# Kernel tuning notes

Measured on AMD Instinct MI355X. Metric: run time of the kernel, lower is better.

The kernel has to match this reference:

```python
import jax, jax.numpy as jnp
import numpy as np

NX, NY = 128, 128
NT = 50
DECAY = 0.1
M1 = M2 = 12
WIDTH = 64


def _spectral(x, w1, w2):
    # x: [B, W, NX, NY]; w1/w2: complex [W, W, M1, M2]
    xf = jnp.fft.rfft2(x)                                   # [B, W, NX, NY//2+1]
    of = jnp.zeros(xf.shape[:2] + (NX, NY // 2 + 1), jnp.complex64)
    of = of.at[:, :, :M1, :M2].set(jnp.einsum('bixy,ioxy->boxy', xf[:, :, :M1, :M2], w1))
    of = of.at[:, :, NX - M1:, :M2].set(jnp.einsum('bixy,ioxy->boxy', xf[:, :, NX - M1:, :M2], w2))
    return jnp.fft.irfft2(of, s=(NX, NY))


def _forward(xyt_q, obs_coords, obs_vals, x_grid, y_grid,
             fc0_w, fc0_b, spec_w1r, spec_w1i, spec_w2r, spec_w2i,
             pw_w, pw_b, fc1_w, fc1_b, fc2_w, fc2_b,
             nb_idx, sensor_iy, sensor_ix, Lx, Ly):
    B, K = nb_idx.shape
    # ---- gather obs, temporal-decay weight, scatter-add into sparse grid ----
    sensor_ids = nb_idx // NT                               # [B, K]
    t_nb = obs_coords[nb_idx, 2]                            # [B, K]
    w = jnp.exp(-DECAY * jnp.abs(t_nb - xyt_q[:, None, 2])) # [B, K]
    vals = obs_vals[nb_idx] * w                             # [B, K]
    lin = sensor_iy[sensor_ids] * NY + sensor_ix[sensor_ids]
    flat = (lin + jnp.arange(B)[:, None] * (NX * NY)).ravel()
    sparse = jnp.zeros(B * NX * NY, obs_vals.dtype).at[flat].add(vals.ravel())
    counts = jnp.zeros(B * NX * NY, obs_vals.dtype).at[flat].add(w.ravel())
    grid = jnp.where(counts > 0, sparse / jnp.maximum(counts, 1e-6), 0.0).reshape(B, NX, NY)
    # ---- FNO core ----
    inp = jnp.stack([grid,
                     jnp.broadcast_to(x_grid, (B, NX, NY)),
                     jnp.broadcast_to(y_grid, (B, NX, NY))], axis=1)  # [B, 3, NX, NY]
    x = jnp.einsum('bcxy,cw->bwxy', inp, fc0_w) + fc0_b[None, :, None, None]
    for i in range(4):
        y = (_spectral(x, spec_w1r[i] + 1j * spec_w1i[i], spec_w2r[i] + 1j * spec_w2i[i])
             + jnp.einsum('bcxy,oc->boxy', x, pw_w[i]) + pw_b[i][None, :, None, None])
        x = jax.nn.gelu(y, approximate=False) if i < 3 else y
    h = jax.nn.gelu(jnp.einsum('bwxy,wf->bxyf', x, fc1_w) + fc1_b, approximate=False)
    field = (jnp.einsum('bxyf,fo->bxyo', h, fc2_w) + fc2_b).transpose(0, 3, 1, 2)  # [B, 3, NX, NY]
    # ---- bilinear sample at query points ----
    x01 = jnp.clip(xyt_q[:, 0] / max(Lx, 1e-6), 0.0, 1.0)
    y01 = jnp.clip(xyt_q[:, 1] / max(Ly, 1e-6), 0.0, 1.0)
    gx = x01 * (NX - 1)
    gy = y01 * (NY - 1)
    x0 = jnp.floor(gx).astype(jnp.int32)
    y0 = jnp.floor(gy).astype(jnp.int32)
    x1 = jnp.minimum(x0 + 1, NX - 1)
    y1 = jnp.minimum(y0 + 1, NY - 1)
    wx = (gx - x0)[:, None]
    wy = (gy - y0)[:, None]
    b = jnp.arange(B)
    f00 = field[b, :, x0, y0]
    f10 = field[b, :, x1, y0]
    f01 = field[b, :, x0, y1]
    f11 = field[b, :, x1, y1]
    top = f00 * (1.0 - wx) + f10 * wx
    bot = f01 * (1.0 - wx) + f11 * wx
    return top * (1.0 - wy) + bot * wy                       # [B, 3]


def setup_inputs() -> dict:
    key = jax.random.key(0)
    ks = jax.random.split(key, 20)
    B, K, NOBS, NS = 64, 64, 50000, 1000
    scale = 1.0 / (WIDTH * WIDTH)
    inp = {
        'xyt_q': jax.random.uniform(ks[0], (B, 3), jnp.float32),
        'obs_coords': jax.random.uniform(ks[1], (NOBS, 3), jnp.float32),
        'obs_vals': jax.random.normal(ks[2], (NOBS,), jnp.float32),
        'x_grid': jax.random.uniform(ks[3], (NX, NY), jnp.float32),
        'y_grid': jax.random.uniform(ks[4], (NX, NY), jnp.float32),
        'fc0_w': jax.random.normal(ks[5], (3, WIDTH), jnp.float32) * 0.3,
        'fc0_b': jnp.zeros((WIDTH,), jnp.float32),
        'spec_w1r': scale * jax.random.uniform(ks[6], (4, WIDTH, WIDTH, M1, M2), jnp.float32),
        'spec_w1i': scale * jax.random.uniform(ks[7], (4, WIDTH, WIDTH, M1, M2), jnp.float32),
        'spec_w2r': scale * jax.random.uniform(ks[8], (4, WIDTH, WIDTH, M1, M2), jnp.float32),
        'spec_w2i': scale * jax.random.uniform(ks[9], (4, WIDTH, WIDTH, M1, M2), jnp.float32),
        'pw_w': jax.random.normal(ks[10], (4, WIDTH, WIDTH), jnp.float32) * (1.0 / np.sqrt(WIDTH)),
        'pw_b': jnp.zeros((4, WIDTH), jnp.float32),
        'fc1_w': jax.random.normal(ks[11], (WIDTH, 128), jnp.float32) * (1.0 / np.sqrt(WIDTH)),
        'fc1_b': jnp.zeros((128,), jnp.float32),
        'fc2_w': jax.random.normal(ks[12], (128, 3), jnp.float32) * (1.0 / np.sqrt(128.0)),
        'fc2_b': jnp.zeros((3,), jnp.float32),
        'nb_idx': jax.random.randint(ks[13], (B, K), 0, NOBS, jnp.int32),
        'sensor_iy': jax.random.randint(ks[14], (NS,), 0, NX, jnp.int32),
        'sensor_ix': jax.random.randint(ks[15], (NS,), 0, NY, jnp.int32),
        'Lx': 1,
        'Ly': 1,
    }
    return inp


def reference(xyt_q, obs_coords, obs_vals, x_grid, y_grid,
              fc0_w, fc0_b, spec_w1r, spec_w1i, spec_w2r, spec_w2i,
              pw_w, pw_b, fc1_w, fc1_b, fc2_w, fc2_b,
              nb_idx, sensor_iy, sensor_ix, Lx, Ly):
    return _forward(xyt_q, obs_coords, obs_vals, x_grid, y_grid,
                    fc0_w, fc0_b, spec_w1r, spec_w1i, spec_w2r, spec_w2i,
                    pw_w, pw_b, fc1_w, fc1_b, fc2_w, fc2_b,
                    nb_idx, sensor_iy, sensor_ix, Lx, Ly)
```

## Files before the change

### kernel.cpp

```cpp
#include <hip/hip_runtime.h>
#include <math.h>

#define NXg 128
#define NYg 128
#define Pg  (NXg*NYg)
#define Bq  64
#define Wd  64
#define NKX 24
#define NMODE (NKX*12)
#define PI2_128 0.04908738521234052f

typedef _Float16 f16x8 __attribute__((ext_vector_type(8)));
typedef _Float16 f16x4 __attribute__((ext_vector_type(4)));
typedef float    f32x4 __attribute__((ext_vector_type(4)));

#define OFF_TC  0
#define OFF_TS  (OFF_TC + 128)
#define F32_END (OFF_TS + 128)
#define H_T1E  0
#define H_T1ET (H_T1E + 32*128)
#define H_A2   (H_T1ET + 128*32)
#define H_PWH  (H_A2 + 48*256)
#define H_T2ET (H_PWH + 4*64*64)
#define H_XFHR (H_T2ET + 128*64)
#define H_XFHI (H_XFHR + 288*4096)
#define H_OFHR (H_XFHI + 288*4096)
#define H_OFHI (H_OFHR + 288*4096)
#define H_WHR  (H_OFHI + 288*4096)
#define H_WHI  (H_WHR + (size_t)4*288*4096)
#define H_YG   (H_WHI + (size_t)4*288*4096)
#define H_X    (H_YG + (size_t)Bq*Wd*128*24)
#define H_U    (H_X + (size_t)Bq*128*128*64)

__device__ __forceinline__ float fast_gelu(float v) {
    float a = fabsf(v) * 0.70710678118654752f;
    float t = 1.f / (1.f + 0.3275911f * a);
    float p = t * (0.254829592f + t * (-0.284496736f + t * (1.421413741f +
              t * (-1.453152027f + t * 1.061405429f))));
    float er = 1.f - p * __expf(-a * a);
    er = copysignf(er, v);
    return 0.5f * v * (1.f + er);
}

__global__ void k_prep(_Float16* T1e_g, _Float16* T1eT_g, _Float16* A2_g,
                       const float* pww, _Float16* PWh, _Float16* T2eT_g,
                       float* Tc, float* Ts,
                       const float* xyt, const float* obs_c, const float* obs_v,
                       const int* nb, const int* siy, const int* six,
                       float* val, float* cnt,
                       const float* w1r, const float* w1i,
                       const float* w2r, const float* w2i,
                       _Float16* Whr, _Float16* Whi) {
    int blk = blockIdx.x;
    if (blk < 64) {
        int t = blk * 256 + threadIdx.x;
        if (t < 32*128) {
            int r = t >> 7, y = t & 127;
            float v = 0.f;
            if (r < 12)      v =  cosf((float)((r * y) & 127) * PI2_128);
            else if (r < 24) v = -sinf((float)(((r-12) * y) & 127) * PI2_128);
            T1e_g[t] = (_Float16)v;
            int y2 = t >> 5, r2 = t & 31;
            float v2 = 0.f;
            if (r2 < 12)      v2 =  cosf((float)((r2 * y2) & 127) * PI2_128);
            else if (r2 < 24) v2 = -sinf((float)(((r2-12) * y2) & 127) * PI2_128);
            T1eT_g[t] = (_Float16)v2;
        }
        if (t < 48*256) {
            int m = t >> 8, k = t & 255;
            int x = k & 127;
            int hi = (k >= 128);
            float v;
            if (m < 24) {
                int kx = (m < 12) ? m : (104 + m);
                float th = (float)((kx * x) & 127) * PI2_128;
                v = hi ? sinf(th) : cosf(th);
            } else {
                int mm = m - 24;
                int kx = (mm < 12) ? mm : (104 + mm);
                float th = (float)((kx * x) & 127) * PI2_128;
                v = hi ? cosf(th) : -sinf(th);
            }
            A2_g[t] = (_Float16)v;
        }
        if (t < 4*64*64) PWh[t] = (_Float16)pww[t];
        if (t < 128*64) {
            int x = t >> 6, k = t & 63;
            float v = 0.f;
            if (k < 24) {
                int kx = (k < 12) ? k : (104 + k);
                v = cosf((float)((kx * x) & 127) * PI2_128);
            } else if (k < 48) {
                int kk = k - 24;
                int kx = (kk < 12) ? kk : (104 + kk);
                v = sinf((float)((kx * x) & 127) * PI2_128);
            }
            T2eT_g[t] = (_Float16)v;
        }
        if (t < 128) {
            float th = (float)t * PI2_128;
            Tc[t] = cosf(th);
            Ts[t] = sinf(th);
        }
    } else if (blk < 80) {
        int t = (blk - 64) * 256 + threadIdx.x;
        int b = t >> 6;
        int id = nb[t];
        int sid = id / 50;
        float tq = xyt[b*3 + 2];
        float w = expf(-0.1f * fabsf(obs_c[id*3 + 2] - tq));
        int lin = siy[sid] * NYg + six[sid];
        atomicAdd(&val[b*Pg + lin], obs_v[id] * w);
        atomicAdd(&cnt[b*Pg + lin], w);
    } else {
        int u = blk - 80;
        int layer = u / 288, mode = u - layer*288;
        int kxi = mode / 12, ky = mode - kxi*12;
        const float *wr, *wi; int kxw;
        if (kxi < 12) { wr = w1r; wi = w1i; kxw = kxi; }
        else          { wr = w2r; wi = w2i; kxw = kxi - 12; }
        size_t obase = (size_t)(layer*288 + mode) * 4096;
        size_t lbase = (size_t)layer * 64*64*144 + (size_t)kxw*12 + ky;
        for (int k = 0; k < 16; k++) {
            int p = k*256 + threadIdx.x;
            int o = p >> 6, i = p & 63;
            size_t widx = lbase + (size_t)(i*64 + o)*144;
            Whr[obase + p] = (_Float16)wr[widx];
            Whi[obase + p] = (_Float16)wi[widx];
        }
    }
}

__device__ __forceinline__ void stageA(const _Float16 (*Xn)[76], const _Float16* __restrict__ T1e_g,
                                       _Float16* __restrict__ Yg, int b, int row, int tid) {
    int wave = tid >> 6, lane = tid & 63;
    int l15 = lane & 15, quad = lane >> 4;
    f16x8 bf[8];
    #pragma unroll
    for (int u = 0; u < 8; u++) {
        int nt2 = u >> 2, q = u & 3;
        bf[u] = *(const f16x8*)&T1e_g[(nt2*16 + l15)*128 + q*32 + quad*8];
    }
    f16x8 af[4];
    #pragma unroll
    for (int q = 0; q < 4; q++)
        #pragma unroll
        for (int j = 0; j < 8; j++)
            af[q][j] = Xn[q*32 + quad*8 + j][wave*16 + l15];
    #pragma unroll
    for (int nt2 = 0; nt2 < 2; nt2++) {
        f32x4 acc = {0.f,0.f,0.f,0.f};
        #pragma unroll
        for (int q = 0; q < 4; q++)
            acc = __builtin_amdgcn_mfma_f32_16x16x32_f16(af[q], bf[nt2*4 + q], acc, 0, 0, 0);
        int t = nt2*16 + l15;
        if (t < 24) {
            #pragma unroll
            for (int r = 0; r < 4; r++) {
                int o = wave*16 + quad*4 + r;
                Yg[((size_t)(b*64 + o)*128 + row)*24 + t] = (_Float16)acc[r];
            }
        }
    }
}

__global__ __launch_bounds__(256) void k_fc0y(const float* __restrict__ val, const float* __restrict__ cnt,
                      const float* __restrict__ xg, const float* __restrict__ yg,
                      const float* __restrict__ w, const float* __restrict__ bb,
                      const _Float16* __restrict__ T1e_g,
                      _Float16* __restrict__ Yg) {
    __shared__ _Float16 Xn[128][76];
    __shared__ float wl[4][64];
    int row = blockIdx.x, b = blockIdx.y;
    int tid = threadIdx.x;
    if (tid < 64) {
        wl[0][tid] = w[tid]; wl[1][tid] = w[64+tid]; wl[2][tid] = w[128+tid]; wl[3][tid] = bb[tid];
    }
    __syncthreads();
    {
        int y = tid & 127, half = tid >> 7;
        int p = row*128 + y;
        float c = cnt[(size_t)b*Pg + p];
        float g = (c > 0.f) ? val[(size_t)b*Pg + p] / fmaxf(c, 1e-6f) : 0.f;
        float a1 = xg[p], a2 = yg[p];
        #pragma unroll
        for (int blk = 0; blk < 4; blk++) {
            f16x8 pk;
            #pragma unroll
            for (int j = 0; j < 8; j++) {
                int o = half*32 + blk*8 + j;
                pk[j] = (_Float16)(g*wl[0][o] + a1*wl[1][o] + a2*wl[2][o] + wl[3][o]);
            }
            *(f16x8*)&Xn[y][half*32 + blk*8] = pk;
        }
    }
    __syncthreads();
    stageA(Xn, T1e_g, Yg, b, row, tid);
}

__global__ __launch_bounds__(256) void k_sB(const _Float16* __restrict__ Yg,
                    const _Float16* __restrict__ A2_g,
                    _Float16* __restrict__ xfhr, _Float16* __restrict__ xfhi) {
    __shared__ _Float16 Ys[28][136];
    int bc = blockIdx.x;
    int tid = threadIdx.x;
    int wave = tid >> 6, lane = tid & 63;
    int l15 = lane & 15, quad = lane >> 4;
    const _Float16* base = Yg + (size_t)bc * 3072;
    for (int i = tid; i < 3072; i += 256) {
        int x = i / 24, t = i - x*24;
        Ys[t][x] = base[i];
    }
    __syncthreads();
    if (wave < 3) {
        f32x4 acc = {0.f,0.f,0.f,0.f};
        #pragma unroll
        for (int q = 0; q < 8; q++) {
            f16x8 a = *(const f16x8*)&A2_g[(size_t)(wave*16 + l15)*256 + q*32 + quad*8];
            const _Float16* brow = (q < 4) ? &Ys[l15][q*32 + quad*8]
                                           : &Ys[12 + l15][(q-4)*32 + quad*8];
            f16x8 bfr = *(const f16x8*)brow;
            acc = __builtin_amdgcn_mfma_f32_16x16x32_f16(a, bfr, acc, 0, 0, 0);
        }
        if (l15 < 12) {
            #pragma unroll
            for (int r = 0; r < 4; r++) {
                int m = wave*16 + quad*4 + r;
                if (m < 24) xfhr[(size_t)(m*12 + l15)*4096 + bc] = (_Float16)acc[r];
                else        xfhi[(size_t)((m-24)*12 + l15)*4096 + bc] = (_Float16)acc[r];
            }
        }
    }
}

__global__ __launch_bounds__(256) void k_s3m(const _Float16* __restrict__ xfhr, const _Float16* __restrict__ xfhi,
                    const _Float16* __restrict__ Whr, const _Float16* __restrict__ Whi,
                    _Float16* __restrict__ ofhr, _Float16* __restrict__ ofhi, int layer) {
    __shared__ _Float16 Xr[64][72], Xi[64][72];
    int mode = blockIdx.x;
    int tid = threadIdx.x;
    int wave = tid >> 6, lane = tid & 63;
    int l15 = lane & 15, quad = lane >> 4;
    const _Float16* pr = xfhr + (size_t)mode * 4096;
    const _Float16* pi = xfhi + (size_t)mode * 4096;
    for (int c8 = tid; c8 < 512; c8 += 256) {
        int b = c8 >> 3, seg = c8 & 7;
        *(f16x8*)&Xr[b][seg*8] = *(const f16x8*)&pr[c8*8];
        *(f16x8*)&Xi[b][seg*8] = *(const f16x8*)&pi[c8*8];
    }
    __syncthreads();
    size_t wb = ((size_t)(layer*288 + mode)*64 + wave*16 + l15) * 64 + quad*8;
    f16x8 wr0 = *(const f16x8*)&Whr[wb];
    f16x8 wr1 = *(const f16x8*)&Whr[wb + 32];
    f16x8 wi0 = *(const f16x8*)&Whi[wb];
    f16x8 wi1 = *(const f16x8*)&Whi[wb + 32];
    #pragma unroll
    for (int mt = 0; mt < 4; mt++) {
        f16x8 xr0 = *(const f16x8*)&Xr[mt*16 + l15][quad*8];
        f16x8 xr1 = *(const f16x8*)&Xr[mt*16 + l15][32 + quad*8];
        f16x8 xi0 = *(const f16x8*)&Xi[mt*16 + l15][quad*8];
        f16x8 xi1 = *(const f16x8*)&Xi[mt*16 + l15][32 + quad*8];
        f16x8 xn0, xn1;
        #pragma unroll
        for (int j = 0; j < 8; j++) { xn0[j] = -xi0[j]; xn1[j] = -xi1[j]; }
        f32x4 cr = {0.f,0.f,0.f,0.f}, ci = {0.f,0.f,0.f,0.f};
        cr = __builtin_amdgcn_mfma_f32_16x16x32_f16(xr0, wr0, cr, 0, 0, 0);
        cr = __builtin_amdgcn_mfma_f32_16x16x32_f16(xr1, wr1, cr, 0, 0, 0);
        cr = __builtin_amdgcn_mfma_f32_16x16x32_f16(xn0, wi0, cr, 0, 0, 0);
        cr = __builtin_amdgcn_mfma_f32_16x16x32_f16(xn1, wi1, cr, 0, 0, 0);
        ci = __builtin_amdgcn_mfma_f32_16x16x32_f16(xr0, wi0, ci, 0, 0, 0);
        ci = __builtin_amdgcn_mfma_f32_16x16x32_f16(xr1, wi1, ci, 0, 0, 0);
        ci = __builtin_amdgcn_mfma_f32_16x16x32_f16(xi0, wr0, ci, 0, 0, 0);
        ci = __builtin_amdgcn_mfma_f32_16x16x32_f16(xi1, wr1, ci, 0, 0, 0);
        #pragma unroll
        for (int r = 0; r < 4; r++) {
            int b = mt*16 + quad*4 + r;
            int o = wave*16 + l15;
            ofhr[(size_t)mode*4096 + b*64 + o] = (_Float16)cr[r];
            ofhi[(size_t)mode*4096 + b*64 + o] = (_Float16)ci[r];
        }
    }
}

__global__ __launch_bounds__(256) void k_sG(const _Float16* __restrict__ ofhr, const _Float16* __restrict__ ofhi,
                    const _Float16* __restrict__ T2eT_g, _Float16* __restrict__ Gh) {
    __shared__ _Float16 As[64][72];
    __shared__ _Float16 Cs[128][72];
    int b = blockIdx.x, t = blockIdx.y;
    int tid = threadIdx.x;
    int wave = tid >> 6, lane = tid & 63;
    int l15 = lane & 15, quad = lane >> 4;
    int ky = (t < 12) ? t : (t - 12);
    float sc = ((ky == 0) ? 1.f : 2.f) * (1.f/16384.f);
    bool isReal = (t < 12);
    for (int i = tid; i < 1536; i += 256) {
        int kxi = i >> 6, o = i & 63;
        size_t idx = (size_t)(kxi*12 + ky)*4096 + b*64 + o;
        float vr = (float)ofhr[idx] * sc, vi = (float)ofhi[idx] * sc;
        As[o][kxi]      = (_Float16)(isReal ? vr : vi);
        As[o][24 + kxi] = (_Float16)(isReal ? -vi : vr);
    }
    for (int i = tid; i < 1024; i += 256)
        As[i >> 4][48 + (i & 15)] = (_Float16)0.f;
    __syncthreads();
    f16x8 a0 = *(const f16x8*)&As[wave*16 + l15][quad*8];
    f16x8 a1 = *(const f16x8*)&As[wave*16 + l15][32 + quad*8];
    #pragma unroll
    for (int nt = 0; nt < 8; nt++) {
        f16x8 b0 = *(const f16x8*)&T2eT_g[(nt*16 + l15)*64 + quad*8];
        f16x8 b1 = *(const f16x8*)&T2eT_g[(nt*16 + l15)*64 + 32 + quad*8];
        f32x4 acc = {0.f,0.f,0.f,0.f};
        acc = __builtin_amdgcn_mfma_f32_16x16x32_f16(a0, b0, acc, 0, 0, 0);
        acc = __builtin_amdgcn_mfma_f32_16x16x32_f16(a1, b1, acc, 0, 0, 0);
        f16x4 pk;
        #pragma unroll
        for (int r = 0; r < 4; r++) pk[r] = (_Float16)acc[r];
        *(f16x4*)&Cs[nt*16 + l15][wave*16 + quad*4] = pk;
    }
    __syncthreads();
    _Float16* outp = Gh + ((size_t)(b*24 + t) << 13);
    float4* o4 = (float4*)outp;
    for (int i = tid; i < 1024; i += 256) {
        int x = i >> 3, seg = i & 7;
        o4[i] = *(const float4*)&Cs[x][seg*8];
    }
}

__global__ __launch_bounds__(256) void k_s45(_Float16* __restrict__ xh,
                    const _Float16* __restrict__ Gh,
                    const _Float16* __restrict__ T1e_g, const _Float16* __restrict__ T1eT_g,
                    const _Float16* __restrict__ PWh,
                    const float* __restrict__ pwb,
                    _Float16* __restrict__ Yg, int layer,
                    const float* __restrict__ xyt, const int* __restrict__ Lx,
                    const float* __restrict__ val, const float* __restrict__ cnt,
                    const float* __restrict__ xg, const float* __restrict__ yg,
                    const float* __restrict__ fc0w, const float* __restrict__ fc0b) {
    __shared__ _Float16 BsT[128][76];
    __shared__ float wl[4][64];
    int row = blockIdx.x, b = blockIdx.y;
    int tid = threadIdx.x;
    int wave = tid >> 6, lane = tid & 63;
    int l15 = lane & 15, quad = lane >> 4;

    _Float16* xrow = xh + (size_t)(b*128 + row) * 8192;

    f16x8 af0 = *(const f16x8*)&PWh[(size_t)(layer*64 + wave*16 + l15)*64 + quad*8];
    f16x8 af1 = *(const f16x8*)&PWh[(size_t)(layer*64 + wave*16 + l15)*64 + 32 + quad*8];
    f16x8 af2;
    #pragma unroll
    for (int j = 0; j < 8; j++) af2[j] = (_Float16)0.f;
    if (quad < 3) {
        const _Float16* gbase = Gh + ((size_t)(b*24 + quad*8)*128 + row)*64 + wave*16 + l15;
        #pragma unroll
        for (int j = 0; j < 8; j++) af2[j] = gbase[(size_t)j * 8192];
    }
    f16x8 b2a[8];
    #pragma unroll
    for (int nt = 0; nt < 8; nt++)
        b2a[nt] = *(const f16x8*)&T1eT_g[(nt*16 + l15)*32 + quad*8];
    float pb[4];
    #pragma unroll
    for (int r = 0; r < 4; r++)
        pb[r] = pwb[layer*64 + wave*16 + quad*4 + r];

    if (layer == 0) {
        if (tid < 64) {
            wl[0][tid] = fc0w[tid]; wl[1][tid] = fc0w[64+tid];
            wl[2][tid] = fc0w[128+tid]; wl[3][tid] = fc0b[tid];
        }
        __syncthreads();
        int y = tid & 127, half = tid >> 7;
        int p = row*128 + y;
        float c = cnt[(size_t)b*Pg + p];
        float g = (c > 0.f) ? val[(size_t)b*Pg + p] / fmaxf(c, 1e-6f) : 0.f;
        float a1 = xg[p], a2 = yg[p];
        #pragma unroll
        for (int blk = 0; blk < 4; blk++) {
            f16x8 pk;
            #pragma unroll
            for (int j = 0; j < 8; j++) {
                int o = half*32 + blk*8 + j;
                pk[j] = (_Float16)(g*wl[0][o] + a1*wl[1][o] + a2*wl[2][o] + wl[3][o]);
            }
            *(f16x8*)&BsT[y][half*32 + blk*8] = pk;
        }
    } else {
        const float4* xr4 = (const float4*)xrow;
        for (int i = tid; i < 1024; i += 256) {
            int y = i >> 3, seg = i & 7;
            *(float4*)&BsT[y][seg*8] = xr4[i];
        }
    }
    __syncthreads();

    f32x4 acc[8];
    #pragma unroll
    for (int nt = 0; nt < 8; nt++) {
        f32x4 a = {0.f,0.f,0.f,0.f};
        f16x8 b0 = *(const f16x8*)&BsT[nt*16 + l15][quad*8];
        f16x8 b1 = *(const f16x8*)&BsT[nt*16 + l15][32 + quad*8];
        a = __builtin_amdgcn_mfma_f32_16x16x32_f16(af0, b0, a, 0, 0, 0);
        a = __builtin_amdgcn_mfma_f32_16x16x32_f16(af1, b1, a, 0, 0, 0);
        a = __builtin_amdgcn_mfma_f32_16x16x32_f16(af2, b2a[nt], a, 0, 0, 0);
        acc[nt] = a;
    }
    __syncthreads();

    #pragma unroll
    for (int nt = 0; nt < 8; nt++) {
        int y = nt*16 + l15;
        f16x4 pk;
        #pragma unroll
        for (int r = 0; r < 4; r++) {
            float v = acc[nt][r] + pb[r];
            pk[r] = (_Float16)fast_gelu(v);
        }
        *(f16x4*)&BsT[y][wave*16 + quad*4] = pk;
    }
    __syncthreads();

    bool store_x = true;
    if (layer == 2) {
        float Lxf = fmaxf((float)Lx[0], 1e-6f);
        float x01 = fminf(fmaxf(xyt[b*3 + 0] / Lxf, 0.f), 1.f);
        float gxp = x01 * (NXg - 1);
        int x0 = (int)floorf(gxp);
        int x1 = min(x0 + 1, NXg - 1);
        store_x = (row == x0) || (row == x1);
    }
    if (store_x) {
        float4* xw4 = (float4*)xrow;
        for (int i = tid; i < 1024; i += 256) {
            int y = i >> 3, seg = i & 7;
            xw4[i] = *(const float4*)&BsT[y][seg*8];
        }
    }
    stageA(BsT, T1e_g, Yg, b, row, tid);
}

__global__ __launch_bounds__(256) void k_final(const _Float16* __restrict__ x,
                    const _Float16* __restrict__ ofhr, const _Float16* __restrict__ ofhi,
                    const float* __restrict__ pw, const float* __restrict__ pwb,
                    const float* __restrict__ fc1w, const float* __restrict__ fc1b,
                    const float* __restrict__ fc2w, const float* __restrict__ fc2b,
                    const float* __restrict__ xyt, const int* __restrict__ Lx, const int* __restrict__ Ly,
                    const float* __restrict__ Tc, const float* __restrict__ Ts,
                    float* __restrict__ out) {
    __shared__ float y4[4][64];
    __shared__ float hh[4][129];
    __shared__ int   pxy[4][2];
    __shared__ float wxy[2];
    __shared__ float tc[128], ts[128];
    int b = blockIdx.x;
    if (threadIdx.x < 128) {
        tc[threadIdx.x] = Tc[threadIdx.x];
        ts[threadIdx.x] = Ts[threadIdx.x];
    }
    if (threadIdx.x == 0) {
        float Lxf = fmaxf((float)Lx[0], 1e-6f);
        float Lyf = fmaxf((float)Ly[0], 1e-6f);
        float x01 = fminf(fmaxf(xyt[b*3 + 0] / Lxf, 0.f), 1.f);
        float y01 = fminf(fmaxf(xyt[b*3 + 1] / Lyf, 0.f), 1.f);
        float gx = x01 * (NXg - 1), gy = y01 * (NYg - 1);
        int x0 = (int)floorf(gx), y0 = (int)floorf(gy);
        int x1 = min(x0 + 1, NXg - 1), y1 = min(y0 + 1, NYg - 1);
        wxy[0] = gx - (float)x0;
        wxy[1] = gy - (float)y0;
        pxy[0][0] = x0; pxy[0][1] = y0;
        pxy[1][0] = x1; pxy[1][1] = y0;
        pxy[2][0] = x0; pxy[2][1] = y1;
        pxy[3][0] = x1; pxy[3][1] = y1;
    }
    __syncthreads();
    {
        int p = threadIdx.x >> 6, o = threadIdx.x & 63;
        int px = pxy[p][0], py = pxy[p][1];
        float gkr[12], gki[12];
        #pragma unroll
        for (int ky = 0; ky < 12; ky++) { gkr[ky] = 0.f; gki[ky] = 0.f; }
        for (int kxi = 0; kxi < 24; kxi++) {
            int kx = (kxi < 12) ? kxi : (104 + kxi);
            int m = (kx * px) & 127;
            float cc = tc[m], ss = ts[m];
            #pragma unroll
            for (int ky = 0; ky < 12; ky++) {
                size_t idx = (size_t)(kxi*12 + ky)*4096 + b*64 + o;
                float a = (float)ofhr[idx], bb = (float)ofhi[idx];
                gkr[ky] += a*cc - bb*ss;
                gki[ky] += a*ss + bb*cc;
            }
        }
        float sp = gkr[0];
        #pragma unroll
        for (int ky = 1; ky < 12; ky++) {
            int m = (ky * py) & 127;
            sp += 2.f * (gkr[ky]*tc[m] - gki[ky]*ts[m]);
        }
        float s = 0.f;
        const _Float16* xb = x + ((size_t)(b*128 + px)*128 + py)*64;
        #pragma unroll 4
        for (int c = 0; c < 64; c++)
            s += pw[3*4096 + o*64 + c] * (float)xb[c];
        y4[p][o] = sp * (1.f/16384.f) + s + pwb[3*64 + o];
    }
    __syncthreads();
    for (int i = threadIdx.x; i < 512; i += 256) {
        int p = i >> 7, f = i & 127;
        float s = fc1b[f];
        #pragma unroll 4
        for (int w = 0; w < 64; w++) s += y4[p][w] * fc1w[w*128 + f];
        hh[p][f] = 0.5f * s * (1.f + erff(s * 0.70710678118654752f));
    }
    __syncthreads();
    if (threadIdx.x < 3) {
        int o3 = threadIdx.x;
        float f4[4];
        #pragma unroll
        for (int p = 0; p < 4; p++) {
            float s = fc2b[o3];
            #pragma unroll 4
            for (int f = 0; f < 128; f++) s += hh[p][f] * fc2w[f*3 + o3];
            f4[p] = s;
        }
        float wx = wxy[0], wy = wxy[1];
        float top = f4[0]*(1.f - wx) + f4[1]*wx;
        float bot = f4[2]*(1.f - wx) + f4[3]*wx;
        out[b*3 + o3] = top*(1.f - wy) + bot*wy;
    }
}

extern "C" void kernel_launch(void* const* d_in, const int* in_sizes, int n_in,
                              void* d_out, int out_size, void* d_ws, size_t ws_size,
                              hipStream_t stream) {
    const float* xyt    = (const float*)d_in[0];
    const float* obs_c  = (const float*)d_in[1];
    const float* obs_v  = (const float*)d_in[2];
    const float* xg     = (const float*)d_in[3];
    const float* yg     = (const float*)d_in[4];
    const float* fc0w   = (const float*)d_in[5];
    const float* fc0b   = (const float*)d_in[6];
    const float* w1r    = (const float*)d_in[7];
    const float* w1i    = (const float*)d_in[8];
    const float* w2r    = (const float*)d_in[9];
    const float* w2i    = (const float*)d_in[10];
    const float* pww    = (const float*)d_in[11];
    const float* pwb    = (const float*)d_in[12];
    const float* fc1w   = (const float*)d_in[13];
    const float* fc1b   = (const float*)d_in[14];
    const float* fc2w   = (const float*)d_in[15];
    const float* fc2b   = (const float*)d_in[16];
    const int*   nb     = (const int*)d_in[17];
    const int*   siy    = (const int*)d_in[18];
    const int*   six    = (const int*)d_in[19];
    const int*   Lx     = (const int*)d_in[20];
    const int*   Ly     = (const int*)d_in[21];
    float* out = (float*)d_out;

    float* W = (float*)d_ws;
    float* Tc  = W + OFF_TC;
    float* Ts  = W + OFF_TS;
    _Float16* Hbase = (_Float16*)(W + F32_END);
    _Float16* T1e_g  = Hbase + H_T1E;
    _Float16* T1eT_g = Hbase + H_T1ET;
    _Float16* A2_g   = Hbase + H_A2;
    _Float16* PWh    = Hbase + H_PWH;
    _Float16* T2eT_g = Hbase + H_T2ET;
    _Float16* xfhr   = Hbase + H_XFHR;
    _Float16* xfhi   = Hbase + H_XFHI;
    _Float16* ofhr   = Hbase + H_OFHR;
    _Float16* ofhi   = Hbase + H_OFHI;
    _Float16* Whr    = Hbase + H_WHR;
    _Float16* Whi    = Hbase + H_WHI;
    _Float16* Yg     = Hbase + H_YG;
    _Float16* xh     = Hbase + H_X;
    float*    val    = (float*)(Hbase + H_U);
    float*    cnt    = val + Bq*Pg;
    _Float16* Gh     = Hbase + H_U;
    _Float16* Gh2    = Hbase + H_U + (size_t)4*Bq*Pg;

    hipMemsetAsync(val, 0, (size_t)2 * Bq * Pg * sizeof(float), stream);

    k_prep<<<1232, 256, 0, stream>>>(T1e_g, T1eT_g, A2_g, pww, PWh, T2eT_g, Tc, Ts,
                                     xyt, obs_c, obs_v, nb, siy, six, val, cnt,
                                     w1r, w1i, w2r, w2i, Whr, Whi);
    k_fc0y<<<dim3(128, Bq), 256, 0, stream>>>(val, cnt, xg, yg, fc0w, fc0b, T1e_g, Yg);

    for (int l = 0; l < 3; l++) {
        k_sB<<<Bq*Wd, 256, 0, stream>>>(Yg, A2_g, xfhr, xfhi);
        k_s3m<<<288, 256, 0, stream>>>(xfhr, xfhi, Whr, Whi, ofhr, ofhi, l);
        k_sG<<<dim3(Bq, 24), 256, 0, stream>>>(ofhr, ofhi, T2eT_g, Gh2);
        k_s45<<<dim3(128, Bq), 256, 0, stream>>>(xh, Gh2, T1e_g, T1eT_g, PWh, pwb, Yg, l,
                                                 xyt, Lx, val, cnt, xg, yg, fc0w, fc0b);
    }
    k_sB<<<Bq*Wd, 256, 0, stream>>>(Yg, A2_g, xfhr, xfhi);
    k_s3m<<<288, 256, 0, stream>>>(xfhr, xfhi, Whr, Whi, ofhr, ofhi, 3);
    k_final<<<Bq, 256, 0, stream>>>(xh, ofhr, ofhi, pww, pwb, fc1w, fc1b, fc2w, fc2b,
                                    xyt, Lx, Ly, Tc, Ts, out);
}
```

Baseline: 745.0 us.

## Process two rows per block in k_s45 and tile spectral weight repack via LDS

k_s45 now handles two grid rows per block, loading the T1e DFT fragments and PW weights once and reusing them across both rows. Results are written to global memory straight from registers instead of through a shared-memory round trip, and the grid is halved. The k_prep weight-conversion path is restructured to stage one output channel's 64x144 slab in LDS, so global reads become coalesced and writes are transposed. This trades higher LDS and register use per block (launch bounds set to 3 blocks per CU) for less redundant loading.

```diff
diff --git a/kernel.cpp b/kernel.cpp
--- a/kernel.cpp
+++ b/kernel.cpp
@@ -51,6 +51,7 @@
                        const float* w1r, const float* w1i,
                        const float* w2r, const float* w2i,
                        _Float16* Whr, _Float16* Whi) {
+    __shared__ _Float16 L[64][146];
     int blk = blockIdx.x;
     if (blk < 64) {
         int t = blk * 256 + threadIdx.x;
@@ -114,33 +115,38 @@
         atomicAdd(&cnt[b*Pg + lin], w);
     } else {
         int u = blk - 80;
-        int layer = u / 288, mode = u - layer*288;
-        int kxi = mode / 12, ky = mode - kxi*12;
-        const float *wr, *wi; int kxw;
-        if (kxi < 12) { wr = w1r; wi = w1i; kxw = kxi; }
-        else          { wr = w2r; wi = w2i; kxw = kxi - 12; }
-        size_t obase = (size_t)(layer*288 + mode) * 4096;
-        size_t lbase = (size_t)layer * 64*64*144 + (size_t)kxw*12 + ky;
-        for (int k = 0; k < 16; k++) {
-            int p = k*256 + threadIdx.x;
-            int o = p >> 6, i = p & 63;
-            size_t widx = lbase + (size_t)(i*64 + o)*144;
-            Whr[obase + p] = (_Float16)wr[widx];
-            Whi[obase + p] = (_Float16)wi[widx];
-        }
-    }
-}
-
-__device__ __forceinline__ void stageA(const _Float16 (*Xn)[76], const _Float16* __restrict__ T1e_g,
-                                       _Float16* __restrict__ Yg, int b, int row, int tid) {
-    int wave = tid >> 6, lane = tid & 63;
+        int layer = u >> 8;
+        int rem = u & 255;
+        int o = rem & 63, ri = (rem >> 6) & 1, half = rem >> 7;
+        const float* src = half ? (ri ? w2i : w2r) : (ri ? w1i : w1r);
+        _Float16* dst = ri ? Whi : Whr;
+        size_t sbase = (size_t)layer * 589824 + (size_t)o * 144;
+        for (int idx = threadIdx.x; idx < 9216; idx += 256) {
+            int i = idx / 144, m = idx - i*144;
+            L[i][m] = (_Float16)src[sbase + (size_t)i*9216 + m];
+        }
+        __syncthreads();
+        size_t obase = ((size_t)(layer*288 + half*144) << 12) + o*64;
+        for (int idx = threadIdx.x; idx < 9216; idx += 256) {
+            int m = idx >> 6, i = idx & 63;
+            dst[obase + ((size_t)m << 12) + i] = L[i][m];
+        }
+    }
+}
+
+__device__ __forceinline__ void stageA_bf(const _Float16* __restrict__ T1e_g, int lane, f16x8* bf) {
     int l15 = lane & 15, quad = lane >> 4;
-    f16x8 bf[8];
     #pragma unroll
     for (int u = 0; u < 8; u++) {
         int nt2 = u >> 2, q = u & 3;
         bf[u] = *(const f16x8*)&T1e_g[(nt2*16 + l15)*128 + q*32 + quad*8];
     }
+}
+
+__device__ __forceinline__ void stageA_core(const _Float16 (*Xn)[76], const f16x8* bf,
+                                            _Float16* __restrict__ Yg, int b, int row, int tid) {
+    int wave = tid >> 6, lane = tid & 63;
+    int l15 = lane & 15, quad = lane >> 4;
     f16x8 af[4];
     #pragma unroll
     for (int q = 0; q < 4; q++)
@@ -162,6 +168,13 @@
             }
         }
     }
+}
+
+__device__ __forceinline__ void stageA(const _Float16 (*Xn)[76], const _Float16* __restrict__ T1e_g,
+                                       _Float16* __restrict__ Yg, int b, int row, int tid) {
+    f16x8 bf[8];
+    stageA_bf(T1e_g, tid & 63, bf);
+    stageA_core(Xn, bf, Yg, b, row, tid);
 }
 
 __global__ __launch_bounds__(256) void k_fc0y(const float* __restrict__ val, const float* __restrict__ cnt,
@@ -326,7 +339,7 @@
     }
 }
 
-__global__ __launch_bounds__(256) void k_s45(_Float16* __restrict__ xh,
+__global__ __launch_bounds__(256, 3) void k_s45(_Float16* __restrict__ xh,
                     const _Float16* __restrict__ Gh,
                     const _Float16* __restrict__ T1e_g, const _Float16* __restrict__ T1eT_g,
                     const _Float16* __restrict__ PWh,
@@ -336,25 +349,30 @@
                     const float* __restrict__ val, const float* __restrict__ cnt,
                     const float* __restrict__ xg, const float* __restrict__ yg,
                     const float* __restrict__ fc0w, const float* __restrict__ fc0b) {
-    __shared__ _Float16 BsT[128][76];
+    __shared__ _Float16 BsT[2][128][76];
     __shared__ float wl[4][64];
-    int row = blockIdx.x, b = blockIdx.y;
+    int rp = blockIdx.x, b = blockIdx.y;
+    int row0 = rp << 1;
     int tid = threadIdx.x;
     int wave = tid >> 6, lane = tid & 63;
     int l15 = lane & 15, quad = lane >> 4;
 
-    _Float16* xrow = xh + (size_t)(b*128 + row) * 8192;
+    f16x8 af2[2];
+    #pragma unroll
+    for (int r2 = 0; r2 < 2; r2++)
+        #pragma unroll
+        for (int j = 0; j < 8; j++) af2[r2][j] = (_Float16)0.f;
+    if (quad < 3) {
+        #pragma unroll
+        for (int r2 = 0; r2 < 2; r2++) {
+            const _Float16* gbase = Gh + ((size_t)(b*24 + quad*8)*128 + row0 + r2)*64 + wave*16 + l15;
+            #pragma unroll
+            for (int j = 0; j < 8; j++) af2[r2][j] = gbase[(size_t)j * 8192];
+        }
+    }
 
     f16x8 af0 = *(const f16x8*)&PWh[(size_t)(layer*64 + wave*16 + l15)*64 + quad*8];
     f16x8 af1 = *(const f16x8*)&PWh[(size_t)(layer*64 + wave*16 + l15)*64 + 32 + quad*8];
-    f16x8 af2;
-    #pragma unroll
-    for (int j = 0; j < 8; j++) af2[j] = (_Float16)0.f;
-    if (quad < 3) {
-        const _Float16* gbase = Gh + ((size_t)(b*24 + quad*8)*128 + row)*64 + wave*16 + l15;
-        #pragma unroll
-        for (int j = 0; j < 8; j++) af2[j] = gbase[(size_t)j * 8192];
-    }
     f16x8 b2a[8];
     #pragma unroll
     for (int nt = 0; nt < 8; nt++)
@@ -371,72 +389,84 @@
         }
         __syncthreads();
         int y = tid & 127, half = tid >> 7;
-        int p = row*128 + y;
-        float c = cnt[(size_t)b*Pg + p];
-        float g = (c > 0.f) ? val[(size_t)b*Pg + p] / fmaxf(c, 1e-6f) : 0.f;
-        float a1 = xg[p], a2 = yg[p];
-        #pragma unroll
-        for (int blk = 0; blk < 4; blk++) {
-            f16x8 pk;
+        #pragma unroll
+        for (int r2 = 0; r2 < 2; r2++) {
+            int p = (row0 + r2)*128 + y;
+            float c = cnt[(size_t)b*Pg + p];
+            float g = (c > 0.f) ? val[(size_t)b*Pg + p] / fmaxf(c, 1e-6f) : 0.f;
+            float a1 = xg[p], a2 = yg[p];
             #pragma unroll
-            for (int j = 0; j < 8; j++) {
-                int o = half*32 + blk*8 + j;
-                pk[j] = (_Float16)(g*wl[0][o] + a1*wl[1][o] + a2*wl[2][o] + wl[3][o]);
-            }
-            *(f16x8*)&BsT[y][half*32 + blk*8] = pk;
+            for (int blk = 0; blk < 4; blk++) {
+                f16x8 pkk;
+                #pragma unroll
+                for (int j = 0; j < 8; j++) {
+                    int o = half*32 + blk*8 + j;
+                    pkk[j] = (_Float16)(g*wl[0][o] + a1*wl[1][o] + a2*wl[2][o] + wl[3][o]);
+                }
+                *(f16x8*)&BsT[r2][y][half*32 + blk*8] = pkk;
+            }
         }
     } else {
-        const float4* xr4 = (const float4*)xrow;
-        for (int i = tid; i < 1024; i += 256) {
-            int y = i >> 3, seg = i & 7;
-            *(float4*)&BsT[y][seg*8] = xr4[i];
-        }
-    }
-    __syncthreads();
-
-    f32x4 acc[8];
-    #pragma unroll
-    for (int nt = 0; nt < 8; nt++) {
-        f32x4 a = {0.f,0.f,0.f,0.f};
-        f16x8 b0 = *(const f16x8*)&BsT[nt*16 + l15][quad*8];
-        f16x8 b1 = *(const f16x8*)&BsT[nt*16 + l15][32 + quad*8];
-        a = __builtin_amdgcn_mfma_f32_16x16x32_f16(af0, b0, a, 0, 0, 0);
-        a = __builtin_amdgcn_mfma_f32_16x16x32_f16(af1, b1, a, 0, 0, 0);
-        a = __builtin_amdgcn_mfma_f32_16x16x32_f16(af2, b2a[nt], a, 0, 0, 0);
-        acc[nt] = a;
-    }
-    __syncthreads();
-
-    #pragma unroll
-    for (int nt = 0; nt < 8; nt++) {
-        int y = nt*16 + l15;
-        f16x4 pk;
-        #pragma unroll
-        for (int r = 0; r < 4; r++) {
-            float v = acc[nt][r] + pb[r];
-            pk[r] = (_Float16)fast_gelu(v);
-        }
-        *(f16x4*)&BsT[y][wave*16 + quad*4] = pk;
-    }
-    __syncthreads();
-
-    bool store_x = true;
+        #pragma unroll
+        for (int r2 = 0; r2 < 2; r2++) {
+            const float4* xr4 = (const float4*)(xh + (size_t)(b*128 + row0 + r2) * 8192);
+            for (int i = tid; i < 1024; i += 256) {
+                int y = i >> 3, seg = i & 7;
+                *(float4*)&BsT[r2][y][seg*8] = xr4[i];
+            }
+        }
+    }
+    __syncthreads();
+
+    f16x4 pk[2][8];
+    #pragma unroll
+    for (int r2 = 0; r2 < 2; r2++) {
+        f32x4 acc[8];
+        #pragma unroll
+        for (int nt = 0; nt < 8; nt++) {
+            f32x4 a = {0.f,0.f,0.f,0.f};
+            f16x8 b0 = *(const f16x8*)&BsT[r2][nt*16 + l15][quad*8];
+            f16x8 b1 = *(const f16x8*)&BsT[r2][nt*16 + l15][32 + quad*8];
+            a = __builtin_amdgcn_mfma_f32_16x16x32_f16(af0, b0, a, 0, 0, 0);
+            a = __builtin_amdgcn_mfma_f32_16x16x32_f16(af1, b1, a, 0, 0, 0);
+            a = __builtin_amdgcn_mfma_f32_16x16x32_f16(af2[r2], b2a[nt], a, 0, 0, 0);
+            acc[nt] = a;
+        }
+        #pragma unroll
+        for (int nt = 0; nt < 8; nt++)
+            #pragma unroll
+            for (int r = 0; r < 4; r++)
+                pk[r2][nt][r] = (_Float16)fast_gelu(acc[nt][r] + pb[r]);
+    }
+    __syncthreads();
+
+    bool st[2] = {true, true};
     if (layer == 2) {
         float Lxf = fmaxf((float)Lx[0], 1e-6f);
         float x01 = fminf(fmaxf(xyt[b*3 + 0] / Lxf, 0.f), 1.f);
         float gxp = x01 * (NXg - 1);
         int x0 = (int)floorf(gxp);
         int x1 = min(x0 + 1, NXg - 1);
-        store_x = (row == x0) || (row == x1);
-    }
-    if (store_x) {
-        float4* xw4 = (float4*)xrow;
-        for (int i = tid; i < 1024; i += 256) {
-            int y = i >> 3, seg = i & 7;
-            xw4[i] = *(const float4*)&BsT[y][seg*8];
-        }
-    }
-    stageA(BsT, T1e_g, Yg, b, row, tid);
+        st[0] = (row0 == x0) || (row0 == x1);
+        st[1] = (row0 + 1 == x0) || (row0 + 1 == x1);
+    }
+    #pragma unroll
+    for (int r2 = 0; r2 < 2; r2++) {
+        _Float16* xrow = xh + (size_t)(b*128 + row0 + r2) * 8192;
+        #pragma unroll
+        for (int nt = 0; nt < 8; nt++) {
+            int y = nt*16 + l15;
+            *(f16x4*)&BsT[r2][y][wave*16 + quad*4] = pk[r2][nt];
+            if (st[r2])
+                *(f16x4*)&xrow[(size_t)y*64 + wave*16 + quad*4] = pk[r2][nt];
+        }
+    }
+    __syncthreads();
+
+    f16x8 bf[8];
+    stageA_bf(T1e_g, lane, bf);
+    stageA_core(BsT[0], bf, Yg, b, row0, tid);
+    stageA_core(BsT[1], bf, Yg, b, row0 + 1, tid);
 }
 
 __global__ __launch_bounds__(256) void k_final(const _Float16* __restrict__ x,
@@ -576,12 +606,11 @@
     _Float16* xh     = Hbase + H_X;
     float*    val    = (float*)(Hbase + H_U);
     float*    cnt    = val + Bq*Pg;
-    _Float16* Gh     = Hbase + H_U;
     _Float16* Gh2    = Hbase + H_U + (size_t)4*Bq*Pg;
 
     hipMemsetAsync(val, 0, (size_t)2 * Bq * Pg * sizeof(float), stream);
 
-    k_prep<<<1232, 256, 0, stream>>>(T1e_g, T1eT_g, A2_g, pww, PWh, T2eT_g, Tc, Ts,
+    k_prep<<<1104, 256, 0, stream>>>(T1e_g, T1eT_g, A2_g, pww, PWh, T2eT_g, Tc, Ts,
                                      xyt, obs_c, obs_v, nb, siy, six, val, cnt,
                                      w1r, w1i, w2r, w2i, Whr, Whi);
     k_fc0y<<<dim3(128, Bq), 256, 0, stream>>>(val, cnt, xg, yg, fc0w, fc0b, T1e_g, Yg);
@@ -590,8 +619,8 @@
         k_sB<<<Bq*Wd, 256, 0, stream>>>(Yg, A2_g, xfhr, xfhi);
         k_s3m<<<288, 256, 0, stream>>>(xfhr, xfhi, Whr, Whi, ofhr, ofhi, l);
         k_sG<<<dim3(Bq, 24), 256, 0, stream>>>(ofhr, ofhi, T2eT_g, Gh2);
-        k_s45<<<dim3(128, Bq), 256, 0, stream>>>(xh, Gh2, T1e_g, T1eT_g, PWh, pwb, Yg, l,
-                                                 xyt, Lx, val, cnt, xg, yg, fc0w, fc0b);
+        k_s45<<<dim3(64, Bq), 256, 0, stream>>>(xh, Gh2, T1e_g, T1eT_g, PWh, pwb, Yg, l,
+                                                xyt, Lx, val, cnt, xg, yg, fc0w, fc0b);
     }
     k_sB<<<Bq*Wd, 256, 0, stream>>>(Yg, A2_g, xfhr, xfhi);
     k_s3m<<<288, 256, 0, stream>>>(xfhr, xfhi, Whr, Whi, ofhr, ofhi, 3);
```

Measured after the change: 918.8 us. 1.23x slower.

## Transpose spectral weights via LDS and reorder Gh for coalesced per-row loads

Applied to the files above, without the earlier changes.

The weight-conversion blocks in k_prep now each load one output channel's full [64 x 144] slab into shared memory with contiguous reads, then write it transposed into the half-precision layout. This replaces the old strided gather and cuts the block count from 1232 to 1104. Separately, k_sG now writes its inverse-transform output in a [b][x][t][64] layout, so each k_s45 block can load its 24x64 slice contiguously into LDS instead of doing strided scalar gathers. The trade-off is extra shared memory and a sync in k_prep, plus a more scattered store pattern in k_sG.

```diff
diff --git a/kernel.cpp b/kernel.cpp
--- a/kernel.cpp
+++ b/kernel.cpp
@@ -51,6 +51,7 @@
                        const float* w1r, const float* w1i,
                        const float* w2r, const float* w2i,
                        _Float16* Whr, _Float16* Whi) {
+    __shared__ _Float16 L[64][146];
     int blk = blockIdx.x;
     if (blk < 64) {
         int t = blk * 256 + threadIdx.x;
@@ -114,19 +115,21 @@
         atomicAdd(&cnt[b*Pg + lin], w);
     } else {
         int u = blk - 80;
-        int layer = u / 288, mode = u - layer*288;
-        int kxi = mode / 12, ky = mode - kxi*12;
-        const float *wr, *wi; int kxw;
-        if (kxi < 12) { wr = w1r; wi = w1i; kxw = kxi; }
-        else          { wr = w2r; wi = w2i; kxw = kxi - 12; }
-        size_t obase = (size_t)(layer*288 + mode) * 4096;
-        size_t lbase = (size_t)layer * 64*64*144 + (size_t)kxw*12 + ky;
-        for (int k = 0; k < 16; k++) {
-            int p = k*256 + threadIdx.x;
-            int o = p >> 6, i = p & 63;
-            size_t widx = lbase + (size_t)(i*64 + o)*144;
-            Whr[obase + p] = (_Float16)wr[widx];
-            Whi[obase + p] = (_Float16)wi[widx];
+        int layer = u >> 8;
+        int rem = u & 255;
+        int o = rem & 63, ri = (rem >> 6) & 1, half = rem >> 7;
+        const float* src = half ? (ri ? w2i : w2r) : (ri ? w1i : w1r);
+        _Float16* dst = ri ? Whi : Whr;
+        size_t sbase = (size_t)layer * 589824 + (size_t)o * 144;
+        for (int idx = threadIdx.x; idx < 9216; idx += 256) {
+            int i = idx / 144, m = idx - i*144;
+            L[i][m] = (_Float16)src[sbase + (size_t)i*9216 + m];
+        }
+        __syncthreads();
+        size_t obase = ((size_t)(layer*288 + half*144) << 12) + o*64;
+        for (int idx = threadIdx.x; idx < 9216; idx += 256) {
+            int m = idx >> 6, i = idx & 63;
+            dst[obase + ((size_t)m << 12) + i] = L[i][m];
         }
     }
 }
@@ -318,11 +321,10 @@
         *(f16x4*)&Cs[nt*16 + l15][wave*16 + quad*4] = pk;
     }
     __syncthreads();
-    _Float16* outp = Gh + ((size_t)(b*24 + t) << 13);
-    float4* o4 = (float4*)outp;
+    float4* o4 = (float4*)Gh;
     for (int i = tid; i < 1024; i += 256) {
         int x = i >> 3, seg = i & 7;
-        o4[i] = *(const float4*)&Cs[x][seg*8];
+        o4[((size_t)((b*128 + x)*24 + t))*8 + seg] = *(const float4*)&Cs[x][seg*8];
     }
 }
 
@@ -337,6 +339,7 @@
                     const float* __restrict__ xg, const float* __restrict__ yg,
                     const float* __restrict__ fc0w, const float* __restrict__ fc0b) {
     __shared__ _Float16 BsT[128][76];
+    __shared__ __align__(16) _Float16 Gs[24][64];
     __shared__ float wl[4][64];
     int row = blockIdx.x, b = blockIdx.y;
     int tid = threadIdx.x;
@@ -345,16 +348,11 @@
 
     _Float16* xrow = xh + (size_t)(b*128 + row) * 8192;
 
+    if (tid < 192)
+        ((float4*)Gs)[tid] = ((const float4*)(Gh + (size_t)(b*128 + row) * 1536))[tid];
+
     f16x8 af0 = *(const f16x8*)&PWh[(size_t)(layer*64 + wave*16 + l15)*64 + quad*8];
     f16x8 af1 = *(const f16x8*)&PWh[(size_t)(layer*64 + wave*16 + l15)*64 + 32 + quad*8];
-    f16x8 af2;
-    #pragma unroll
-    for (int j = 0; j < 8; j++) af2[j] = (_Float16)0.f;
-    if (quad < 3) {
-        const _Float16* gbase = Gh + ((size_t)(b*24 + quad*8)*128 + row)*64 + wave*16 + l15;
-        #pragma unroll
-        for (int j = 0; j < 8; j++) af2[j] = gbase[(size_t)j * 8192];
-    }
     f16x8 b2a[8];
     #pragma unroll
     for (int nt = 0; nt < 8; nt++)
@@ -393,6 +391,11 @@
         }
     }
     __syncthreads();
+
+    f16x8 af2;
+    #pragma unroll
+    for (int j = 0; j < 8; j++)
+        af2[j] = (quad < 3) ? Gs[quad*8 + j][wave*16 + l15] : (_Float16)0.f;
 
     f32x4 acc[8];
     #pragma unroll
@@ -576,12 +579,11 @@
     _Float16* xh     = Hbase + H_X;
     float*    val    = (float*)(Hbase + H_U);
     float*    cnt    = val + Bq*Pg;
-    _Float16* Gh     = Hbase + H_U;
     _Float16* Gh2    = Hbase + H_U + (size_t)4*Bq*Pg;
 
     hipMemsetAsync(val, 0, (size_t)2 * Bq * Pg * sizeof(float), stream);
 
-    k_prep<<<1232, 256, 0, stream>>>(T1e_g, T1eT_g, A2_g, pww, PWh, T2eT_g, Tc, Ts,
+    k_prep<<<1104, 256, 0, stream>>>(T1e_g, T1eT_g, A2_g, pww, PWh, T2eT_g, Tc, Ts,
                                      xyt, obs_c, obs_v, nb, siy, six, val, cnt,
                                      w1r, w1i, w2r, w2i, Whr, Whi);
     k_fc0y<<<dim3(128, Bq), 256, 0, stream>>>(val, cnt, xg, yg, fc0w, fc0b, T1e_g, Yg);
```

Result: faster. 690.5 us (-7.3%).
